# Optimization experiments

Measured on AMD Instinct MI355X. Metric: run time of the kernel, lower is better.

## Reference

```python
import jax, jax.numpy as jnp
import numpy as np

B, W, H, L, D = 4, 32, 32, 32, 256
K, S, V = 24, 16384, 8  # heads, selected positions per head, logits per head
N = B * W * H * L


def setup_inputs() -> dict:
    key = jax.random.key(0)
    k1, k2, k3, k4, k5 = jax.random.split(key, 5)
    block_type_grid = jax.random.randint(k1, (B, W, H, L), 0, 800, dtype=jnp.int32)
    features = jax.random.normal(k2, (B, W, H, L, D), dtype=jnp.float32)
    mask_idx = jax.random.randint(k3, (K, S), 0, N, dtype=jnp.int32)
    head_weights = jax.random.normal(k4, (K, D, V), dtype=jnp.float32) * (1.0 / np.sqrt(D))
    head_bias = jax.random.normal(k5, (K, V), dtype=jnp.float32) * 0.01
    return {
        "block_type_grid": block_type_grid,
        "features": features,
        "mask_idx": mask_idx,
        "head_weights": head_weights,
        "head_bias": head_bias,
    }


def reference(block_type_grid, features, mask_idx, head_weights, head_bias):
    # Flatten spatial grid: (B,W,H,L,D) -> (N,D)
    feats_flat = features.reshape(-1, D)
    # Grouped boolean-mask gather (as fixed-size index gather): (K,S,D)
    gathered = feats_flat[mask_idx]
    # Per-head small Linear: logits[k,s,v] = gathered[k,s,:] @ W[k,:,v] + b[k,v]
    logits = jnp.einsum('ksd,kdv->ksv', gathered, head_weights) + head_bias[:, None, :]
    return logits
```

## Files before the change

### kernel.cpp

```cpp
#include <hip/hip_runtime.h>


#define KH 24
#define SS 16384
#define VV 8
#define DD 256
#define PITCH 264

typedef short bf16x8 __attribute__((ext_vector_type(8)));
typedef float f32x4  __attribute__((ext_vector_type(4)));

__device__ __forceinline__ short f32_bf16_rne(float f) {
    unsigned u = __builtin_bit_cast(unsigned, f);
    u = (u + 0x7FFFu + ((u >> 16) & 1u)) >> 16;
    return (short)u;
}

__device__ __forceinline__ int pack_bf16x2(float lo, float hi) {
    unsigned ulo = __builtin_bit_cast(unsigned, lo) + 0x8000u;
    unsigned uhi = __builtin_bit_cast(unsigned, hi) + 0x8000u;
    return __builtin_amdgcn_perm(uhi, ulo, 0x07060302);
}

__global__ __launch_bounds__(256) void attr_decoder_kernel(
    const float* __restrict__ feats,
    const int*   __restrict__ mask_idx,
    const float* __restrict__ head_w,
    const float* __restrict__ head_b,
    float*       __restrict__ out)
{
    __shared__ short lds[4][16 * PITCH];

    const int lane  = threadIdx.x & 63;
    const int wv    = threadIdx.x >> 6;
    const int k     = blockIdx.x >> 7;
    const int chunk = blockIdx.x & 127;
    const int n     = lane & 15;
    const int q     = lane >> 4;

    const float* Wk = head_w + (size_t)k * (DD * VV);
    bf16x8 Bf[8];
#pragma unroll
    for (int t = 0; t < 8; ++t) {
#pragma unroll
        for (int j = 0; j < 8; ++j) {
            const int kd = t * 32 + q * 8 + j;
            Bf[t][j] = (n < VV) ? f32_bf16_rne(Wk[kd * VV + n]) : (short)0;
        }
    }
    const float bn = (n < VV) ? head_b[k * VV + n] : 0.f;

    const float4* feats4 = (const float4*)feats;
    const int s_base = chunk * 128 + wv * 32;
    const int* mi = mask_idx + k * SS + s_base;
    float* outp = out + ((size_t)k * SS + s_base) * VV;
    short* alds = lds[wv];

    int rows[32];
#pragma unroll
    for (int c = 0; c < 8; ++c) {
        const int4 r = ((const int4*)mi)[c];
        rows[4 * c + 0] = r.x; rows[4 * c + 1] = r.y;
        rows[4 * c + 2] = r.z; rows[4 * c + 3] = r.w;
    }

    float4 f[16];
#pragma unroll
    for (int j = 0; j < 16; ++j)
        f[j] = feats4[(size_t)rows[j] * 64 + lane];

#pragma unroll
    for (int tile = 0; tile < 2; ++tile) {
#pragma unroll
        for (int j = 0; j < 16; ++j) {
            int2 p;
            p.x = pack_bf16x2(f[j].x, f[j].y);
            p.y = pack_bf16x2(f[j].z, f[j].w);
            *(int2*)(alds + j * PITCH + lane * 4) = p;
        }
        if (tile == 0) {
#pragma unroll
            for (int j = 0; j < 16; ++j)
                f[j] = feats4[(size_t)rows[16 + j] * 64 + lane];
        }
        f32x4 acc = {0.f, 0.f, 0.f, 0.f};
#pragma unroll
        for (int t = 0; t < 8; ++t) {
            const bf16x8 a = *(const bf16x8*)(alds + n * PITCH + t * 32 + q * 8);
            acc = __builtin_amdgcn_mfma_f32_16x16x32_bf16(a, Bf[t], acc, 0, 0, 0);
        }
        if (n < VV) {
            float* op = outp + (size_t)(tile * 16 + q * 4) * VV + n;
            op[0]  = acc[0] + bn;
            op[8]  = acc[1] + bn;
            op[16] = acc[2] + bn;
            op[24] = acc[3] + bn;
        }
    }
}

extern "C" void kernel_launch(void* const* d_in, const int* in_sizes, int n_in,
                              void* d_out, int out_size, void* d_ws, size_t ws_size,
                              hipStream_t stream) {
    const float* feats    = (const float*)d_in[1];
    const int*   mask_idx = (const int*)  d_in[2];
    const float* head_w   = (const float*)d_in[3];
    const float* head_b   = (const float*)d_in[4];
    float* out = (float*)d_out;

    dim3 grid(KH * 128);
    dim3 block(256);
    attr_decoder_kernel<<<grid, block, 0, stream>>>(feats, mask_idx, head_w, head_b, out);
}
```

Baseline: 256.3 us.

## Load gathered rows directly into MFMA operand layout, drop LDS staging

Each lane now loads its own gathered feature row segment straight from global memory in the layout the MFMA A operand needs, converts it to bf16 in registers, and skips the shared-memory transpose. Each wave processes four 16-row tiles in a non-unrolled loop, so the grid is halved, and launch bounds ask for 8 blocks per CU. This removes LDS traffic and the large per-thread register prefetch in exchange for less coalesced per-lane 32-byte loads and less memory-level parallelism per wave, which higher occupancy has to make up.

```diff
diff --git a/kernel.cpp b/kernel.cpp
--- a/kernel.cpp
+++ b/kernel.cpp
@@ -5,10 +5,10 @@
 #define SS 16384
 #define VV 8
 #define DD 256
-#define PITCH 264
 
 typedef short bf16x8 __attribute__((ext_vector_type(8)));
 typedef float f32x4  __attribute__((ext_vector_type(4)));
+typedef int   i32x4  __attribute__((ext_vector_type(4)));
 
 __device__ __forceinline__ short f32_bf16_rne(float f) {
     unsigned u = __builtin_bit_cast(unsigned, f);
@@ -16,25 +16,23 @@
     return (short)u;
 }
 
-__device__ __forceinline__ int pack_bf16x2(float lo, float hi) {
+__device__ __forceinline__ unsigned pack_bf16x2(float lo, float hi) {
     unsigned ulo = __builtin_bit_cast(unsigned, lo) + 0x8000u;
     unsigned uhi = __builtin_bit_cast(unsigned, hi) + 0x8000u;
     return __builtin_amdgcn_perm(uhi, ulo, 0x07060302);
 }
 
-__global__ __launch_bounds__(256) void attr_decoder_kernel(
+__global__ __launch_bounds__(256, 8) void attr_decoder_kernel(
     const float* __restrict__ feats,
     const int*   __restrict__ mask_idx,
     const float* __restrict__ head_w,
     const float* __restrict__ head_b,
     float*       __restrict__ out)
 {
-    __shared__ short lds[4][16 * PITCH];
-
     const int lane  = threadIdx.x & 63;
     const int wv    = threadIdx.x >> 6;
-    const int k     = blockIdx.x >> 7;
-    const int chunk = blockIdx.x & 127;
+    const int k     = blockIdx.x >> 6;
+    const int chunk = blockIdx.x & 63;
     const int n     = lane & 15;
     const int q     = lane >> 4;
 
@@ -50,43 +48,29 @@
     }
     const float bn = (n < VV) ? head_b[k * VV + n] : 0.f;
 
-    const float4* feats4 = (const float4*)feats;
-    const int s_base = chunk * 128 + wv * 32;
+    const int s_base = chunk * 256 + wv * 64;
     const int* mi = mask_idx + k * SS + s_base;
     float* outp = out + ((size_t)k * SS + s_base) * VV;
-    short* alds = lds[wv];
 
-    int rows[32];
+    int r[4];
 #pragma unroll
-    for (int c = 0; c < 8; ++c) {
-        const int4 r = ((const int4*)mi)[c];
-        rows[4 * c + 0] = r.x; rows[4 * c + 1] = r.y;
-        rows[4 * c + 2] = r.z; rows[4 * c + 3] = r.w;
-    }
+    for (int tile = 0; tile < 4; ++tile)
+        r[tile] = mi[tile * 16 + n];
 
-    float4 f[16];
-#pragma unroll
-    for (int j = 0; j < 16; ++j)
-        f[j] = feats4[(size_t)rows[j] * 64 + lane];
-
-#pragma unroll
-    for (int tile = 0; tile < 2; ++tile) {
-#pragma unroll
-        for (int j = 0; j < 16; ++j) {
-            int2 p;
-            p.x = pack_bf16x2(f[j].x, f[j].y);
-            p.y = pack_bf16x2(f[j].z, f[j].w);
-            *(int2*)(alds + j * PITCH + lane * 4) = p;
-        }
-        if (tile == 0) {
-#pragma unroll
-            for (int j = 0; j < 16; ++j)
-                f[j] = feats4[(size_t)rows[16 + j] * 64 + lane];
-        }
+#pragma unroll 1
+    for (int tile = 0; tile < 4; ++tile) {
+        const float* p = feats + (size_t)r[tile] * DD + q * 8;
         f32x4 acc = {0.f, 0.f, 0.f, 0.f};
 #pragma unroll
         for (int t = 0; t < 8; ++t) {
-            const bf16x8 a = *(const bf16x8*)(alds + n * PITCH + t * 32 + q * 8);
+            const float4 a0 = *(const float4*)(p + t * 32);
+            const float4 a1 = *(const float4*)(p + t * 32 + 4);
+            i32x4 ai;
+            ai[0] = (int)pack_bf16x2(a0.x, a0.y);
+            ai[1] = (int)pack_bf16x2(a0.z, a0.w);
+            ai[2] = (int)pack_bf16x2(a1.x, a1.y);
+            ai[3] = (int)pack_bf16x2(a1.z, a1.w);
+            const bf16x8 a = __builtin_bit_cast(bf16x8, ai);
             acc = __builtin_amdgcn_mfma_f32_16x16x32_bf16(a, Bf[t], acc, 0, 0, 0);
         }
         if (n < VV) {
@@ -108,7 +92,7 @@
     const float* head_b   = (const float*)d_in[4];
     float* out = (float*)d_out;
 
-    dim3 grid(KH * 128);
+    dim3 grid(KH * 64);
     dim3 block(256);
     attr_decoder_kernel<<<grid, block, 0, stream>>>(feats, mask_idx, head_w, head_b, out);
 }
```

New measurement: 246.7 us. 1.04x faster.
